# Kernel optimization log

Measured on AMD Instinct MI355X. Metric: run time of the kernel, lower is better.

Reference implementation:

```python
import jax, jax.numpy as jnp
import numpy as np

B, T, N, D, H = 16, 12, 325, 64, 4
E = 2600
NEG_SLOPE = 0.2
LN_EPS = 1e-5
SM_EPS = 1e-16


def setup_inputs() -> dict:
    key = jax.random.key(0)
    ks = jax.random.split(key, 8)
    x = jax.random.normal(ks[0], (B, T, N, D), dtype=jnp.float32)
    edge_index = jax.random.randint(ks[1], (2, E), 0, N, dtype=jnp.int64)
    W = jax.random.normal(ks[2], (D, H, D), dtype=jnp.float32) * 0.05   # lin weight, [in, heads, out]
    att_src = jax.random.normal(ks[3], (H, D), dtype=jnp.float32) * 0.05
    att_dst = jax.random.normal(ks[4], (H, D), dtype=jnp.float32) * 0.05
    bias = jnp.zeros((D,), dtype=jnp.float32)
    gamma = jnp.ones((D,), dtype=jnp.float32)
    beta = jnp.zeros((D,), dtype=jnp.float32)
    return {"x": x, "W": W, "att_src": att_src, "att_dst": att_dst,
            "bias": bias, "gamma": gamma, "beta": beta, "edge_index": edge_index}


def reference(x, W, att_src, att_dst, bias, gamma, beta, edge_index):
    b, t, n, d = x.shape
    bt = b * t
    xb = x.reshape(bt, n, d)

    # add self-loops (GATConv default add_self_loops=True)
    loops = jnp.arange(n, dtype=edge_index.dtype)
    src = jnp.concatenate([edge_index[0], loops])  # message source j
    dst = jnp.concatenate([edge_index[1], loops])  # message target i

    # per-head linear projection, node axis leading for segment ops: [N, BT, H, D]
    xp = jnp.einsum('bnd,dhf->nbhf', xb, W)

    a_src = jnp.einsum('nbhf,hf->nbh', xp, att_src)  # [N, BT, H]
    a_dst = jnp.einsum('nbhf,hf->nbh', xp, att_dst)

    alpha = a_src[src] + a_dst[dst]                  # [Etot, BT, H]
    alpha = jnp.where(alpha >= 0, alpha, NEG_SLOPE * alpha)

    # segment softmax over incoming edges of each dst node
    m = jax.ops.segment_max(alpha, dst, num_segments=n)        # [N, BT, H]
    e = jnp.exp(alpha - m[dst])
    s = jax.ops.segment_sum(e, dst, num_segments=n)            # [N, BT, H]
    coef = e / (s[dst] + SM_EPS)                               # [Etot, BT, H]

    # weighted scatter-sum aggregation
    msgs = coef[..., None] * xp[src]                           # [Etot, BT, H, D]
    out = jax.ops.segment_sum(msgs, dst, num_segments=n)       # [N, BT, H, D]

    out = out.mean(axis=2) + bias                              # concat=False -> head mean; [N, BT, D]
    out = out.transpose(1, 0, 2).reshape(b, t, n, d)

    # residual + LayerNorm
    y = x + out
    mu = y.mean(axis=-1, keepdims=True)
    var = y.var(axis=-1, keepdims=True)
    return (y - mu) * jax.lax.rsqrt(var + LN_EPS) * gamma + beta
```

## Files before the change

kernel.cpp:

```cpp
#include <hip/hip_runtime.h>

#define Nn 325
#define Dd 64
#define Hh 4
#define Ee 2600
#define BT 192
#define ETOT (Ee+Nn)
#define NROWS (BT*Nn)

typedef __attribute__((ext_vector_type(8))) short bf16x8;
typedef __attribute__((ext_vector_type(4))) float f32x4;

static __device__ __forceinline__ short f2bf(float f) {
    union { float f; unsigned u; } v; v.f = f;
    unsigned r = v.u + 0x7fffu + ((v.u >> 16) & 1u);
    return (short)(r >> 16);
}
static __device__ __forceinline__ float bf_lo(unsigned p) {
    union { unsigned u; float f; } v; v.u = p << 16; return v.f;
}
static __device__ __forceinline__ float bf_hi(unsigned p) {
    union { unsigned u; float f; } v; v.u = p & 0xffff0000u; return v.f;
}

__global__ __launch_bounds__(256) void k_proj(
    const float* __restrict__ x, const float* __restrict__ W,
    const float* __restrict__ att_src, const float* __restrict__ att_dst,
    unsigned short* __restrict__ xp, float* __restrict__ asrc,
    float* __restrict__ adst)
{
    const int t = threadIdx.x;
    const int w = t >> 6;
    const int lane = t & 63;
    const int q = lane >> 4;
    const int l16 = lane & 15;
    const int g0 = blockIdx.x * 16;

    bf16x8 afr[2];
    #pragma unroll
    for (int kk = 0; kk < 2; ++kk) {
        const float* xr = x + (size_t)(g0 + l16) * Dd + kk * 32 + q * 8;
        float4 a0 = *(const float4*)xr;
        float4 a1 = *(const float4*)(xr + 4);
        afr[kk][0]=f2bf(a0.x); afr[kk][1]=f2bf(a0.y); afr[kk][2]=f2bf(a0.z); afr[kk][3]=f2bf(a0.w);
        afr[kk][4]=f2bf(a1.x); afr[kk][5]=f2bf(a1.y); afr[kk][6]=f2bf(a1.z); afr[kk][7]=f2bf(a1.w);
    }
    bf16x8 bfr[4][2];
    #pragma unroll
    for (int tl = 0; tl < 4; ++tl) {
        const int col = w * 64 + tl * 16 + l16;
        #pragma unroll
        for (int kk = 0; kk < 2; ++kk)
            #pragma unroll
            for (int j = 0; j < 8; ++j)
                bfr[tl][kk][j] = f2bf(W[(size_t)(kk * 32 + q * 8 + j) * 256 + col]);
    }

    f32x4 acc[4];
    #pragma unroll
    for (int tl = 0; tl < 4; ++tl) {
        acc[tl] = (f32x4){0.f, 0.f, 0.f, 0.f};
        acc[tl] = __builtin_amdgcn_mfma_f32_16x16x32_bf16(afr[0], bfr[tl][0], acc[tl], 0, 0, 0);
        acc[tl] = __builtin_amdgcn_mfma_f32_16x16x32_bf16(afr[1], bfr[tl][1], acc[tl], 0, 0, 0);
    }

    float avs[4], avd[4];
    #pragma unroll
    for (int tl = 0; tl < 4; ++tl) {
        avs[tl] = att_src[w * 64 + tl * 16 + l16];
        avd[tl] = att_dst[w * 64 + tl * 16 + l16];
    }
    #pragma unroll
    for (int r = 0; r < 4; ++r) {
        float ps = 0.f, pd = 0.f;
        #pragma unroll
        for (int tl = 0; tl < 4; ++tl) {
            ps = fmaf(acc[tl][r], avs[tl], ps);
            pd = fmaf(acc[tl][r], avd[tl], pd);
        }
        #pragma unroll
        for (int off = 1; off < 16; off <<= 1) {
            ps += __shfl_xor(ps, off);
            pd += __shfl_xor(pd, off);
        }
        if (l16 == 0) {
            asrc[(size_t)(g0 + q * 4 + r) * Hh + w] = ps;
            adst[(size_t)(g0 + q * 4 + r) * Hh + w] = pd;
        }
    }

    __shared__ unsigned short ldsXP[16][264];
    #pragma unroll
    for (int tl = 0; tl < 4; ++tl)
        #pragma unroll
        for (int r = 0; r < 4; ++r)
            ldsXP[q * 4 + r][(tl * 16 + l16) * 4 + w] = (unsigned short)f2bf(acc[tl][r]);
    __syncthreads();
    #pragma unroll
    for (int c = 0; c < 2; ++c) {
        int idx = t + c * 256;
        int row = idx >> 5;
        int off = (idx & 31) * 8;
        uint4 v = *(const uint4*)&ldsXP[row][off];
        *(uint4*)(xp + (size_t)(g0 + row) * 256 + off) = v;
    }
}

__global__ void k_csr(const int* __restrict__ ei,
                      int* __restrict__ offs, int* __restrict__ elist)
{
    __shared__ int cnt[Nn + 1];
    __shared__ int cur[Nn];
    const int t = threadIdx.x;
    for (int i = t; i <= Nn; i += 256) cnt[i] = 0;
    __syncthreads();
    for (int e = t; e < ETOT; e += 256) {
        int d = (e < Ee) ? ei[Ee + e] : (e - Ee);
        atomicAdd(&cnt[d + 1], 1);
    }
    __syncthreads();
    if (t == 0) {
        int s = 0;
        for (int i = 0; i <= Nn; ++i) { s += cnt[i]; cnt[i] = s; }
    }
    __syncthreads();
    for (int i = t; i <= Nn; i += 256) offs[i] = cnt[i];
    for (int i = t; i < Nn; i += 256) cur[i] = cnt[i];
    __syncthreads();
    for (int e = t; e < ETOT; e += 256) {
        int s, d;
        if (e < Ee) { s = ei[e]; d = ei[Ee + e]; }
        else        { s = e - Ee; d = e - Ee; }
        int slot = atomicAdd(&cur[d], 1);
        elist[slot] = s;
    }
}

__global__ __launch_bounds__(256) void k_aggr(
    const unsigned short* __restrict__ xp, const float* __restrict__ asrc,
    const float* __restrict__ adst, const int* __restrict__ offs,
    const int* __restrict__ elist, const float* __restrict__ x,
    const float* __restrict__ bias, const float* __restrict__ gamma,
    const float* __restrict__ beta, float* __restrict__ out)
{
    const int wave = threadIdx.x >> 6;
    const int lane = threadIdx.x & 63;
    const int p = blockIdx.x * 4 + wave;
    const int n = p % Nn;
    const int bt = p / Nn;
    const int btN = bt * Nn;
    const int row_i = btN + n;
    const int o0 = offs[n];
    const int deg = offs[n + 1] - o0;
    const int el = lane >> 2;
    const int h  = lane & 3;
    const float adi_h = adst[(size_t)row_i * Hh + h];

    __shared__ float coefS[4][64];
    __shared__ int   jS[4][16];

    float m = -1e30f, s = 0.f;
    for (int base = 0; base < deg; base += 16) {
        const int e = base + el;
        if (e < deg) {
            const int j = elist[o0 + e];
            float a = asrc[(size_t)(btN + j) * Hh + h] + adi_h;
            a = (a >= 0.f) ? a : 0.2f * a;
            float M = fmaxf(m, a);
            s = s * __expf(m - M) + __expf(a - M);
            m = M;
        }
    }
    #pragma unroll
    for (int off = 4; off < 64; off <<= 1) {
        float m2 = __shfl_xor(m, off);
        float s2 = __shfl_xor(s, off);
        float M = fmaxf(m, m2);
        s = s * __expf(m - M) + s2 * __expf(m2 - M);
        m = M;
    }
    const float inv_s = 1.f / (s + 1e-16f);

    float acc = 0.f;
    for (int base = 0; base < deg; base += 16) {
        const int e = base + el;
        float c = 0.f; int j = 0;
        if (e < deg) {
            j = elist[o0 + e];
            float a = asrc[(size_t)(btN + j) * Hh + h] + adi_h;
            a = (a >= 0.f) ? a : 0.2f * a;
            c = __expf(a - m) * inv_s;
        }
        coefS[wave][lane] = c;
        if (h == 0) jS[wave][el] = j;
        const int lim = min(16, deg - base);
        for (int e2 = 0; e2 < lim; ++e2) {
            const unsigned short* xpr = xp + (size_t)(btN + jS[wave][e2]) * 256 + lane * 4;
            uint2 raw = *(const uint2*)xpr;
            const float4 c4 = *(const float4*)&coefS[wave][e2 * 4];
            acc = fmaf(c4.x, bf_lo(raw.x), acc);
            acc = fmaf(c4.y, bf_hi(raw.x), acc);
            acc = fmaf(c4.z, bf_lo(raw.y), acc);
            acc = fmaf(c4.w, bf_hi(raw.y), acc);
        }
    }

    float om = acc * (1.f / Hh) + bias[lane];
    float y = x[(size_t)row_i * Dd + lane] + om;
    float s1 = y, s2v = y * y;
    #pragma unroll
    for (int off = 32; off; off >>= 1) {
        s1  += __shfl_xor(s1, off);
        s2v += __shfl_xor(s2v, off);
    }
    float mu  = s1 * (1.f / Dd);
    float var = s2v * (1.f / Dd) - mu * mu;
    float r = rsqrtf(var + 1e-5f);
    out[(size_t)row_i * Dd + lane] = (y - mu) * r * gamma[lane] + beta[lane];
}

extern "C" void kernel_launch(void* const* d_in, const int* in_sizes, int n_in,
                              void* d_out, int out_size, void* d_ws, size_t ws_size,
                              hipStream_t stream)
{
    const float* x       = (const float*)d_in[0];
    const float* W       = (const float*)d_in[1];
    const float* att_src = (const float*)d_in[2];
    const float* att_dst = (const float*)d_in[3];
    const float* bias    = (const float*)d_in[4];
    const float* gamma   = (const float*)d_in[5];
    const float* beta    = (const float*)d_in[6];
    const int*   ei      = (const int*)d_in[7];

    unsigned short* xp = (unsigned short*)d_ws;
    float* asrc  = (float*)(xp + (size_t)NROWS * 256);
    float* adst  = asrc + (size_t)NROWS * Hh;
    int*   offs  = (int*)(adst + (size_t)NROWS * Hh);
    int*   elist = offs + (Nn + 1);
    float* out   = (float*)d_out;

    hipLaunchKernelGGL(k_csr, dim3(1), dim3(256), 0, stream, ei, offs, elist);
    hipLaunchKernelGGL(k_proj, dim3(NROWS / 16), dim3(256), 0, stream,
                       x, W, att_src, att_dst, xp, asrc, adst);
    hipLaunchKernelGGL(k_aggr, dim3(NROWS / 4), dim3(256), 0, stream,
                       xp, asrc, adst, offs, elist, x, bias, gamma, beta, out);
}
```

Baseline: 164.6 us.

## Pre-pack bf16 weights, double rows per proj block, XCD-aware wide-load aggregation

A new prep kernel converts W once into a per-thread packed bf16 fragment layout, so k_proj loads weights as vector reads instead of strided scalar float loads plus conversions. k_proj now handles 32 rows per block so each weight load is reused twice. The CSR prefix sum becomes a wave-level shuffle scan instead of a serial loop. k_aggr maps blocks so each XCD works on a contiguous set of bt slices for L2 locality, reads 16-byte xp chunks with two edges per wave in flight, passes neighbor indices by shuffle instead of LDS, and uses vectorized epilogue loads and stores. The costs are an extra kernel launch and some idle waves in padded blocks.

```diff
diff --git a/kernel.cpp b/kernel.cpp
--- a/kernel.cpp
+++ b/kernel.cpp
@@ -23,8 +23,19 @@
     union { unsigned u; float f; } v; v.u = p & 0xffff0000u; return v.f;
 }
 
+__global__ __launch_bounds__(256) void k_prep(
+    const float* __restrict__ W, unsigned short* __restrict__ Wt)
+{
+    const int f = blockIdx.x * 256 + threadIdx.x;
+    const int t = f >> 6, idx = f & 63;
+    const int tl = idx >> 4, kk = (idx >> 3) & 1, j = idx & 7;
+    const int w = t >> 6, lane = t & 63;
+    const int q = lane >> 4, l16 = lane & 15;
+    Wt[f] = (unsigned short)f2bf(W[(size_t)(kk * 32 + q * 8 + j) * 256 + w * 64 + tl * 16 + l16]);
+}
+
 __global__ __launch_bounds__(256) void k_proj(
-    const float* __restrict__ x, const float* __restrict__ W,
+    const float* __restrict__ x, const unsigned short* __restrict__ Wt,
     const float* __restrict__ att_src, const float* __restrict__ att_dst,
     unsigned short* __restrict__ xp, float* __restrict__ asrc,
     float* __restrict__ adst)
@@ -34,35 +45,39 @@
     const int lane = t & 63;
     const int q = lane >> 4;
     const int l16 = lane & 15;
-    const int g0 = blockIdx.x * 16;
-
-    bf16x8 afr[2];
-    #pragma unroll
-    for (int kk = 0; kk < 2; ++kk) {
-        const float* xr = x + (size_t)(g0 + l16) * Dd + kk * 32 + q * 8;
-        float4 a0 = *(const float4*)xr;
-        float4 a1 = *(const float4*)(xr + 4);
-        afr[kk][0]=f2bf(a0.x); afr[kk][1]=f2bf(a0.y); afr[kk][2]=f2bf(a0.z); afr[kk][3]=f2bf(a0.w);
-        afr[kk][4]=f2bf(a1.x); afr[kk][5]=f2bf(a1.y); afr[kk][6]=f2bf(a1.z); afr[kk][7]=f2bf(a1.w);
-    }
+    const int g0 = blockIdx.x * 32;
+
     bf16x8 bfr[4][2];
-    #pragma unroll
-    for (int tl = 0; tl < 4; ++tl) {
-        const int col = w * 64 + tl * 16 + l16;
+    const bf16x8* wtp = (const bf16x8*)(Wt + (size_t)t * 64);
+    #pragma unroll
+    for (int tl = 0; tl < 4; ++tl)
         #pragma unroll
         for (int kk = 0; kk < 2; ++kk)
-            #pragma unroll
-            for (int j = 0; j < 8; ++j)
-                bfr[tl][kk][j] = f2bf(W[(size_t)(kk * 32 + q * 8 + j) * 256 + col]);
-    }
-
-    f32x4 acc[4];
-    #pragma unroll
-    for (int tl = 0; tl < 4; ++tl) {
-        acc[tl] = (f32x4){0.f, 0.f, 0.f, 0.f};
-        acc[tl] = __builtin_amdgcn_mfma_f32_16x16x32_bf16(afr[0], bfr[tl][0], acc[tl], 0, 0, 0);
-        acc[tl] = __builtin_amdgcn_mfma_f32_16x16x32_bf16(afr[1], bfr[tl][1], acc[tl], 0, 0, 0);
-    }
+            bfr[tl][kk] = wtp[tl * 2 + kk];
+
+    bf16x8 afr[2][2];
+    #pragma unroll
+    for (int rt = 0; rt < 2; ++rt)
+        #pragma unroll
+        for (int kk = 0; kk < 2; ++kk) {
+            const float* xr = x + (size_t)(g0 + rt * 16 + l16) * Dd + kk * 32 + q * 8;
+            float4 a0 = *(const float4*)xr;
+            float4 a1 = *(const float4*)(xr + 4);
+            afr[rt][kk][0]=f2bf(a0.x); afr[rt][kk][1]=f2bf(a0.y);
+            afr[rt][kk][2]=f2bf(a0.z); afr[rt][kk][3]=f2bf(a0.w);
+            afr[rt][kk][4]=f2bf(a1.x); afr[rt][kk][5]=f2bf(a1.y);
+            afr[rt][kk][6]=f2bf(a1.z); afr[rt][kk][7]=f2bf(a1.w);
+        }
+
+    f32x4 acc[2][4];
+    #pragma unroll
+    for (int rt = 0; rt < 2; ++rt)
+        #pragma unroll
+        for (int tl = 0; tl < 4; ++tl) {
+            acc[rt][tl] = (f32x4){0.f, 0.f, 0.f, 0.f};
+            acc[rt][tl] = __builtin_amdgcn_mfma_f32_16x16x32_bf16(afr[rt][0], bfr[tl][0], acc[rt][tl], 0, 0, 0);
+            acc[rt][tl] = __builtin_amdgcn_mfma_f32_16x16x32_bf16(afr[rt][1], bfr[tl][1], acc[rt][tl], 0, 0, 0);
+        }
 
     float avs[4], avd[4];
     #pragma unroll
@@ -71,34 +86,39 @@
         avd[tl] = att_dst[w * 64 + tl * 16 + l16];
     }
     #pragma unroll
-    for (int r = 0; r < 4; ++r) {
-        float ps = 0.f, pd = 0.f;
-        #pragma unroll
-        for (int tl = 0; tl < 4; ++tl) {
-            ps = fmaf(acc[tl][r], avs[tl], ps);
-            pd = fmaf(acc[tl][r], avd[tl], pd);
-        }
-        #pragma unroll
-        for (int off = 1; off < 16; off <<= 1) {
-            ps += __shfl_xor(ps, off);
-            pd += __shfl_xor(pd, off);
-        }
-        if (l16 == 0) {
-            asrc[(size_t)(g0 + q * 4 + r) * Hh + w] = ps;
-            adst[(size_t)(g0 + q * 4 + r) * Hh + w] = pd;
-        }
-    }
-
-    __shared__ unsigned short ldsXP[16][264];
-    #pragma unroll
-    for (int tl = 0; tl < 4; ++tl)
-        #pragma unroll
-        for (int r = 0; r < 4; ++r)
-            ldsXP[q * 4 + r][(tl * 16 + l16) * 4 + w] = (unsigned short)f2bf(acc[tl][r]);
-    __syncthreads();
-    #pragma unroll
-    for (int c = 0; c < 2; ++c) {
-        int idx = t + c * 256;
+    for (int rt = 0; rt < 2; ++rt)
+        #pragma unroll
+        for (int r = 0; r < 4; ++r) {
+            float ps = 0.f, pd = 0.f;
+            #pragma unroll
+            for (int tl = 0; tl < 4; ++tl) {
+                ps = fmaf(acc[rt][tl][r], avs[tl], ps);
+                pd = fmaf(acc[rt][tl][r], avd[tl], pd);
+            }
+            #pragma unroll
+            for (int off = 1; off < 16; off <<= 1) {
+                ps += __shfl_xor(ps, off);
+                pd += __shfl_xor(pd, off);
+            }
+            if (l16 == 0) {
+                asrc[(size_t)(g0 + rt * 16 + q * 4 + r) * Hh + w] = ps;
+                adst[(size_t)(g0 + rt * 16 + q * 4 + r) * Hh + w] = pd;
+            }
+        }
+
+    __shared__ unsigned short ldsXP[32][264];
+    #pragma unroll
+    for (int rt = 0; rt < 2; ++rt)
+        #pragma unroll
+        for (int tl = 0; tl < 4; ++tl)
+            #pragma unroll
+            for (int r = 0; r < 4; ++r)
+                ldsXP[rt * 16 + q * 4 + r][(tl * 16 + l16) * 4 + w] =
+                    (unsigned short)f2bf(acc[rt][tl][r]);
+    __syncthreads();
+    #pragma unroll
+    for (int c = 0; c < 4; ++c) {
+        int idx = c * 256 + t;
         int row = idx >> 5;
         int off = (idx & 31) * 8;
         uint4 v = *(const uint4*)&ldsXP[row][off];
@@ -112,6 +132,7 @@
     __shared__ int cnt[Nn + 1];
     __shared__ int cur[Nn];
     const int t = threadIdx.x;
+    const int lane = t & 63;
     for (int i = t; i <= Nn; i += 256) cnt[i] = 0;
     __syncthreads();
     for (int e = t; e < ETOT; e += 256) {
@@ -119,9 +140,20 @@
         atomicAdd(&cnt[d + 1], 1);
     }
     __syncthreads();
-    if (t == 0) {
-        int s = 0;
-        for (int i = 0; i <= Nn; ++i) { s += cnt[i]; cnt[i] = s; }
+    if (t < 64) {
+        int run = 0;
+        for (int c = 0; c < 6; ++c) {
+            int i = c * 64 + lane;
+            int v = (i <= Nn) ? cnt[i] : 0;
+            #pragma unroll
+            for (int off = 1; off < 64; off <<= 1) {
+                int u = __shfl_up(v, off);
+                if (lane >= off) v += u;
+            }
+            v += run;
+            if (i <= Nn) cnt[i] = v;
+            run = __shfl(v, 63);
+        }
     }
     __syncthreads();
     for (int i = t; i <= Nn; i += 256) offs[i] = cnt[i];
@@ -145,9 +177,11 @@
 {
     const int wave = threadIdx.x >> 6;
     const int lane = threadIdx.x & 63;
-    const int p = blockIdx.x * 4 + wave;
-    const int n = p % Nn;
-    const int bt = p / Nn;
+    const int xcd = blockIdx.x & 7;
+    const int s_  = blockIdx.x >> 3;
+    const int bt  = xcd * 24 + s_ / 82;
+    const int n   = (s_ % 82) * 4 + wave;
+    if (n >= Nn) return;
     const int btN = bt * Nn;
     const int row_i = btN + n;
     const int o0 = offs[n];
@@ -157,7 +191,6 @@
     const float adi_h = adst[(size_t)row_i * Hh + h];
 
     __shared__ float coefS[4][64];
-    __shared__ int   jS[4][16];
 
     float m = -1e30f, s = 0.f;
     for (int base = 0; base < deg; base += 16) {
@@ -181,7 +214,10 @@
     }
     const float inv_s = 1.f / (s + 1e-16f);
 
-    float acc = 0.f;
+    const int half = lane >> 5;
+    const int fl = lane & 31;
+    float a0=0,a1=0,a2=0,a3=0,a4=0,a5=0,a6=0,a7=0;
+    const unsigned short* xpbt = xp + (size_t)btN * 256;
     for (int base = 0; base < deg; base += 16) {
         const int e = base + el;
         float c = 0.f; int j = 0;
@@ -192,31 +228,49 @@
             c = __expf(a - m) * inv_s;
         }
         coefS[wave][lane] = c;
-        if (h == 0) jS[wave][el] = j;
         const int lim = min(16, deg - base);
-        for (int e2 = 0; e2 < lim; ++e2) {
-            const unsigned short* xpr = xp + (size_t)(btN + jS[wave][e2]) * 256 + lane * 4;
-            uint2 raw = *(const uint2*)xpr;
-            const float4 c4 = *(const float4*)&coefS[wave][e2 * 4];
-            acc = fmaf(c4.x, bf_lo(raw.x), acc);
-            acc = fmaf(c4.y, bf_hi(raw.x), acc);
-            acc = fmaf(c4.z, bf_lo(raw.y), acc);
-            acc = fmaf(c4.w, bf_hi(raw.y), acc);
-        }
-    }
-
-    float om = acc * (1.f / Hh) + bias[lane];
-    float y = x[(size_t)row_i * Dd + lane] + om;
-    float s1 = y, s2v = y * y;
-    #pragma unroll
-    for (int off = 32; off; off >>= 1) {
+        for (int i2 = 0; 2 * i2 < lim; ++i2) {
+            const int eh = 2 * i2 + half;
+            const int jb = __shfl(j, eh * 4);
+            const float4 c4 = *(const float4*)&coefS[wave][eh * 4];
+            uint4 raw = *(const uint4*)(xpbt + (size_t)jb * 256 + fl * 8);
+            a0 = fmaf(c4.x, bf_lo(raw.x), a0);
+            a1 = fmaf(c4.y, bf_hi(raw.x), a1);
+            a2 = fmaf(c4.z, bf_lo(raw.y), a2);
+            a3 = fmaf(c4.w, bf_hi(raw.y), a3);
+            a4 = fmaf(c4.x, bf_lo(raw.z), a4);
+            a5 = fmaf(c4.y, bf_hi(raw.z), a5);
+            a6 = fmaf(c4.z, bf_lo(raw.w), a6);
+            a7 = fmaf(c4.w, bf_hi(raw.w), a7);
+        }
+    }
+    a0 += __shfl_xor(a0, 32); a1 += __shfl_xor(a1, 32);
+    a2 += __shfl_xor(a2, 32); a3 += __shfl_xor(a3, 32);
+    a4 += __shfl_xor(a4, 32); a5 += __shfl_xor(a5, 32);
+    a6 += __shfl_xor(a6, 32); a7 += __shfl_xor(a7, 32);
+
+    const int f0 = fl * 2;
+    float2 bi = *(const float2*)(bias + f0);
+    float2 xv = *(const float2*)(x + (size_t)row_i * Dd + f0);
+    float y0 = xv.x + (a0 + a1 + a2 + a3) * 0.25f + bi.x;
+    float y1 = xv.y + (a4 + a5 + a6 + a7) * 0.25f + bi.y;
+    float s1 = y0 + y1, s2v = y0 * y0 + y1 * y1;
+    #pragma unroll
+    for (int off = 1; off < 32; off <<= 1) {
         s1  += __shfl_xor(s1, off);
         s2v += __shfl_xor(s2v, off);
     }
     float mu  = s1 * (1.f / Dd);
     float var = s2v * (1.f / Dd) - mu * mu;
     float r = rsqrtf(var + 1e-5f);
-    out[(size_t)row_i * Dd + lane] = (y - mu) * r * gamma[lane] + beta[lane];
+    if (half == 0) {
+        float2 ga = *(const float2*)(gamma + f0);
+        float2 be = *(const float2*)(beta + f0);
+        float2 o;
+        o.x = (y0 - mu) * r * ga.x + be.x;
+        o.y = (y1 - mu) * r * ga.y + be.y;
+        *(float2*)(out + (size_t)row_i * Dd + f0) = o;
+    }
 }
 
 extern "C" void kernel_launch(void* const* d_in, const int* in_sizes, int n_in,
@@ -233,15 +287,17 @@
     const int*   ei      = (const int*)d_in[7];
 
     unsigned short* xp = (unsigned short*)d_ws;
-    float* asrc  = (float*)(xp + (size_t)NROWS * 256);
+    unsigned short* Wt = xp + (size_t)NROWS * 256;
+    float* asrc  = (float*)(Wt + 16384);
     float* adst  = asrc + (size_t)NROWS * Hh;
     int*   offs  = (int*)(adst + (size_t)NROWS * Hh);
     int*   elist = offs + (Nn + 1);
     float* out   = (float*)d_out;
 
     hipLaunchKernelGGL(k_csr, dim3(1), dim3(256), 0, stream, ei, offs, elist);
-    hipLaunchKernelGGL(k_proj, dim3(NROWS / 16), dim3(256), 0, stream,
-                       x, W, att_src, att_dst, xp, asrc, adst);
-    hipLaunchKernelGGL(k_aggr, dim3(NROWS / 4), dim3(256), 0, stream,
+    hipLaunchKernelGGL(k_prep, dim3(64), dim3(256), 0, stream, W, Wt);
+    hipLaunchKernelGGL(k_proj, dim3(NROWS / 32), dim3(256), 0, stream,
+                       x, Wt, att_src, att_dst, xp, asrc, adst);
+    hipLaunchKernelGGL(k_aggr, dim3(8 * 24 * 82), dim3(256), 0, stream,
                        xp, asrc, adst, offs, elist, x, bias, gamma, beta, out);
 }
```

Measured after the change: 154.7 us. 6.0% less time.
